# Kernel tuning notes

Hardware: AMD Instinct MI355X
Metric: run time of the kernel (lower is better)

Reference implementation:

```python
import jax, jax.numpy as jnp
import numpy as np

B, D, CTX, H = 262144, 16, 128, 192
IN_DIM = D + CTX + 1  # 145


def _linear_init(k, fan_in, fan_out):
    bound = 1.0 / np.sqrt(fan_in)
    kw, kb = jax.random.split(k)
    W = jax.random.uniform(kw, (fan_in, fan_out), jnp.float32, -bound, bound)
    b = jax.random.uniform(kb, (fan_out,), jnp.float32, -bound, bound)
    return W, b


def setup_inputs() -> dict:
    key = jax.random.key(0)
    ks = jax.random.split(key, 7)
    W1, b1 = _linear_init(ks[0], IN_DIM, H)
    W2, b2 = _linear_init(ks[1], H, H)
    W3, b3 = _linear_init(ks[2], H, D)
    return {
        "t": jax.random.uniform(ks[3], (), jnp.float32),
        "y": jax.random.normal(ks[4], (B, D), jnp.float32),
        "logp": jnp.zeros((B,), jnp.float32),
        "h": jax.random.normal(ks[5], (B, CTX), jnp.float32),
        "eps": jax.random.normal(ks[6], (B, D), jnp.float32),
        "W1": W1, "b1": b1, "W2": W2, "b2": b2, "W3": W3, "b3": b3,
    }


def _mlp(x, W1, b1, W2, b2, W3, b3):
    # 3-layer MLP, exact (erf) GELU as torch.nn.GELU default
    x = jax.nn.gelu(x @ W1 + b1, approximate=False)
    x = jax.nn.gelu(x @ W2 + b2, approximate=False)
    return x @ W3 + b3


def reference(t, y, logp, h, eps, W1, b1, W2, b2, W3, b3):
    Bsz = y.shape[0]
    t_feat = jnp.ones((Bsz, 1), y.dtype) * t

    def f_of_y(yy):
        inp = jnp.concatenate([yy, h, t_feat], axis=1)  # (B, D+CTX+1)
        return _mlp(inp, W1, b1, W2, b2, W3, b3)  # (B, D)

    # Hutchinson: torch computes g = J^T eps then (g*eps).sum(1) = eps^T J^T eps,
    # which per-row equals eps^T J eps = dot(eps, J eps). Forward-mode JVP computes
    # f and J eps in one fused pass (same math, no explicit backward graph).
    f, Jeps = jax.jvp(f_of_y, (y,), (eps,))
    trace = jnp.sum(Jeps * eps, axis=1)  # (B,)
    dlogp = -trace
    dh = jnp.zeros_like(h)
    return (f, dlogp, dh)
```

## Files before the change

### kernel.cpp

```cpp
#include <hip/hip_runtime.h>
#include <hip/hip_bf16.h>
#include <math.h>

#define B_TOTAL 262144
#define D 16
#define CTX 128
#define H 192
#define IN_DIM 145
#define KP1 160
#define M 32
#define BLOCK 256

typedef __attribute__((ext_vector_type(8))) short bf16x8;
typedef __attribute__((ext_vector_type(4))) float f32x4;
typedef __attribute__((ext_vector_type(4))) unsigned short u16x4;

#define MFMA(a, b, c) __builtin_amdgcn_mfma_f32_16x16x32_bf16((a), (b), (c), 0, 0, 0)

__device__ __forceinline__ unsigned short f2bf_rne(float f) {
    unsigned u = __builtin_bit_cast(unsigned, f);
    u += 0x7FFFu + ((u >> 16) & 1u);
    return (unsigned short)(u >> 16);
}
__device__ __forceinline__ void split2(float v, unsigned short& hi, unsigned short& lo) {
    unsigned u = __builtin_bit_cast(unsigned, v);
    hi = (unsigned short)(u >> 16);
    float hf = __builtin_bit_cast(float, u & 0xFFFF0000u);
    lo = f2bf_rne(v - hf);
}
__device__ __forceinline__ void gelu_pair(float x, float& a, float& gp) {
    float s   = x * x;
    float e   = __expf(-0.5f * s);
    float az  = fabsf(x) * 0.70710678118654752f;
    float t   = __builtin_amdgcn_rcpf(fmaf(0.3275911f, az, 1.0f));
    float p   = t * (0.254829592f + t * (-0.284496736f + t * (1.421413741f +
                t * (-1.453152027f + t * 1.061405429f))));
    float erfv = __builtin_copysignf(1.0f - p * e, x);
    float phi  = fmaf(0.5f, erfv, 0.5f);
    gp = fmaf(0.39894228040143268f * x, e, phi);
    a  = x * phi;
}

__global__ void prep_weights(const float* __restrict__ W1,
                             const float* __restrict__ W2,
                             const float* __restrict__ W3,
                             unsigned short* __restrict__ wt)
{
    int i = blockIdx.x * 256 + threadIdx.x;
    if (i < H * KP1) {
        int n = i / KP1, kp = i % KP1;
        float v = 0.0f;
        if (kp < 16)       v = W1[kp * H + n];
        else if (kp == 16) v = W1[144 * H + n];
        else if (kp >= 32) v = W1[(kp - 16) * H + n];
        wt[i] = f2bf_rne(v);
        return;
    }
    i -= H * KP1;
    if (i < H * H) {
        int n = i / H, k = i % H;
        wt[30720 + i] = f2bf_rne(W2[k * H + n]);
        return;
    }
    i -= H * H;
    if (i < D * H) {
        int n = i / H, k = i % H;
        wt[67584 + i] = f2bf_rne(W3[k * D + n]);
    }
}

__global__ __launch_bounds__(BLOCK, 4) void odefunc_mfma(
    const float* __restrict__ t_ptr,
    const float* __restrict__ y,
    const float* __restrict__ h,
    const float* __restrict__ eps,
    const float* __restrict__ b1,
    const float* __restrict__ b2,
    const float* __restrict__ b3,
    const unsigned short* __restrict__ wt,
    float* __restrict__ out_f,
    float* __restrict__ out_dlogp,
    float* __restrict__ out_dh)
{
    __shared__ __align__(16) unsigned char smem[25600];
    unsigned short (*Xh)[168] = (unsigned short (*)[168])(smem);
    unsigned short (*Xl)[40]  = (unsigned short (*)[40])(smem + 10752);
    unsigned short (*Th)[40]  = (unsigned short (*)[40])(smem + 13312);
    unsigned short (*Tl)[40]  = (unsigned short (*)[40])(smem + 15872);
    unsigned short (*A)[200]  = (unsigned short (*)[200])(smem);
    unsigned short (*U)[200]  = (unsigned short (*)[200])(smem + 12800);

    const int tid  = threadIdx.x;
    const int lane = tid & 63;
    const int wv   = tid >> 6;
    const int quad = lane >> 4;
    const int l16  = lane & 15;
    const size_t r0 = (size_t)blockIdx.x * M;

    const unsigned short* Wt1 = wt;
    const unsigned short* Wt2 = wt + 30720;
    const unsigned short* Wt3 = wt + 67584;

    {
        float4 z4 = {0.f, 0.f, 0.f, 0.f};
        #pragma unroll
        for (int i = 0; i < 4; ++i) {
            int idx = tid + i * BLOCK;
            int r = idx >> 5, c4 = (idx & 31) * 4;
            *(float4*)(out_dh + (r0 + r) * CTX + c4) = z4;
        }
    }

    {
        int task = tid >> 7, idx = tid & 127;
        int r = idx >> 2, d4 = (idx & 3) * 4;
        const float* src = task ? eps : y;
        float4 v = *(const float4*)(src + (r0 + r) * D + d4);
        ushort4 hi, lo;
        split2(v.x, hi.x, lo.x); split2(v.y, hi.y, lo.y);
        split2(v.z, hi.z, lo.z); split2(v.w, hi.w, lo.w);
        if (task == 0) { *(ushort4*)&Xh[r][d4] = hi; *(ushort4*)&Xl[r][d4] = lo; }
        else           { *(ushort4*)&Th[r][d4] = hi; *(ushort4*)&Tl[r][d4] = lo; }
    }
    if (tid < M) {
        int r = tid;
        float tv = t_ptr[0];
        unsigned short thi, tlo;
        split2(tv, thi, tlo);
        ushort4 z4 = {0, 0, 0, 0};
        ushort4 t4 = {thi, 0, 0, 0};
        ushort4 l4 = {tlo, 0, 0, 0};
        *(ushort4*)&Xh[r][16] = t4; *(ushort4*)&Xh[r][20] = z4;
        *(ushort4*)&Xh[r][24] = z4; *(ushort4*)&Xh[r][28] = z4;
        *(ushort4*)&Xl[r][16] = l4; *(ushort4*)&Xl[r][20] = z4;
        *(ushort4*)&Xl[r][24] = z4; *(ushort4*)&Xl[r][28] = z4;
        *(ushort4*)&Th[r][16] = z4; *(ushort4*)&Th[r][20] = z4;
        *(ushort4*)&Th[r][24] = z4; *(ushort4*)&Th[r][28] = z4;
        *(ushort4*)&Tl[r][16] = z4; *(ushort4*)&Tl[r][20] = z4;
        *(ushort4*)&Tl[r][24] = z4; *(ushort4*)&Tl[r][28] = z4;
    }
    #pragma unroll
    for (int i = 0; i < 4; ++i) {
        int idx = tid + i * BLOCK;
        int r = idx >> 5, c4 = (idx & 31) * 4;
        float4 v = *(const float4*)(h + (r0 + r) * CTX + c4);
        ushort4 hv = { f2bf_rne(v.x), f2bf_rne(v.y), f2bf_rne(v.z), f2bf_rne(v.w) };
        *(ushort4*)&Xh[r][32 + c4] = hv;
    }
    __syncthreads();

    const f32x4 zf = {0.f, 0.f, 0.f, 0.f};

    f32x4 z[2][3], u[2][3];
    #pragma unroll
    for (int rt = 0; rt < 2; ++rt)
        #pragma unroll
        for (int j = 0; j < 3; ++j) { z[rt][j] = zf; u[rt][j] = zf; }

    bf16x8 w1f[3][5];
    #pragma unroll
    for (int j = 0; j < 3; ++j) {
        int n = (wv * 3 + j) * 16 + l16;
        #pragma unroll
        for (int kc = 0; kc < 5; ++kc)
            w1f[j][kc] = *(const bf16x8*)(Wt1 + n * KP1 + kc * 32 + quad * 8);
    }
    #pragma unroll
    for (int kc = 0; kc < 5; ++kc)
        #pragma unroll
        for (int rt = 0; rt < 2; ++rt) {
            bf16x8 ah = *(const bf16x8*)&Xh[rt * 16 + l16][kc * 32 + quad * 8];
            #pragma unroll
            for (int j = 0; j < 3; ++j) z[rt][j] = MFMA(w1f[j][kc], ah, z[rt][j]);
        }
    #pragma unroll
    for (int rt = 0; rt < 2; ++rt) {
        int m = rt * 16 + l16;
        bf16x8 al = *(const bf16x8*)&Xl[m][quad * 8];
        bf16x8 th = *(const bf16x8*)&Th[m][quad * 8];
        bf16x8 tl = *(const bf16x8*)&Tl[m][quad * 8];
        #pragma unroll
        for (int j = 0; j < 3; ++j) {
            z[rt][j] = MFMA(w1f[j][0], al, z[rt][j]);
            u[rt][j] = MFMA(w1f[j][0], th, u[rt][j]);
            u[rt][j] = MFMA(w1f[j][0], tl, u[rt][j]);
        }
    }
    __syncthreads();
    #pragma unroll
    for (int j = 0; j < 3; ++j) {
        int n4 = (wv * 3 + j) * 16 + quad * 4;
        f32x4 bb4 = *(const f32x4*)(b1 + n4);
        #pragma unroll
        for (int rt = 0; rt < 2; ++rt) {
            int m = rt * 16 + l16;
            u16x4 a4, u4;
            #pragma unroll
            for (int rg = 0; rg < 4; ++rg) {
                float x = z[rt][j][rg] + bb4[rg];
                float a, gp; gelu_pair(x, a, gp);
                a4[rg] = f2bf_rne(a);
                u4[rg] = f2bf_rne(u[rt][j][rg] * gp);
            }
            *(u16x4*)&A[m][n4] = a4;
            *(u16x4*)&U[m][n4] = u4;
        }
    }
    __syncthreads();

    f32x4 z2[2][3], u2[2][3];
    #pragma unroll
    for (int rt = 0; rt < 2; ++rt)
        #pragma unroll
        for (int j = 0; j < 3; ++j) { z2[rt][j] = zf; u2[rt][j] = zf; }

    bf16x8 w2f[3][6];
    #pragma unroll
    for (int j = 0; j < 3; ++j) {
        int n = (wv * 3 + j) * 16 + l16;
        #pragma unroll
        for (int kc = 0; kc < 6; ++kc)
            w2f[j][kc] = *(const bf16x8*)(Wt2 + n * H + kc * 32 + quad * 8);
    }
    #pragma unroll
    for (int kc = 0; kc < 6; ++kc)
        #pragma unroll
        for (int rt = 0; rt < 2; ++rt) {
            int m = rt * 16 + l16, o = kc * 32 + quad * 8;
            bf16x8 av = *(const bf16x8*)&A[m][o];
            bf16x8 uv = *(const bf16x8*)&U[m][o];
            #pragma unroll
            for (int j = 0; j < 3; ++j) {
                z2[rt][j] = MFMA(w2f[j][kc], av, z2[rt][j]);
                u2[rt][j] = MFMA(w2f[j][kc], uv, u2[rt][j]);
            }
        }
    __syncthreads();
    #pragma unroll
    for (int j = 0; j < 3; ++j) {
        int n4 = (wv * 3 + j) * 16 + quad * 4;
        f32x4 bb4 = *(const f32x4*)(b2 + n4);
        #pragma unroll
        for (int rt = 0; rt < 2; ++rt) {
            int m = rt * 16 + l16;
            u16x4 a4, u4;
            #pragma unroll
            for (int rg = 0; rg < 4; ++rg) {
                float x = z2[rt][j][rg] + bb4[rg];
                float a, gp; gelu_pair(x, a, gp);
                a4[rg] = f2bf_rne(a);
                u4[rg] = f2bf_rne(u2[rt][j][rg] * gp);
            }
            *(u16x4*)&A[m][n4] = a4;
            *(u16x4*)&U[m][n4] = u4;
        }
    }
    __syncthreads();

    {
        const int strm = wv & 1, r3 = wv >> 1;
        const unsigned short (*P)[200] = strm ? U : A;

        bf16x8 w3f[6];
        #pragma unroll
        for (int kc = 0; kc < 6; ++kc)
            w3f[kc] = *(const bf16x8*)(Wt3 + l16 * H + kc * 32 + quad * 8);

        f32x4 acc = zf;
        #pragma unroll
        for (int kc = 0; kc < 6; ++kc) {
            bf16x8 xv = *(const bf16x8*)&P[r3 * 16 + l16][kc * 32 + quad * 8];
            acc = MFMA(w3f[kc], xv, acc);
        }

        const int m = r3 * 16 + l16;
        if (strm == 0) {
            f32x4 bb4 = *(const f32x4*)(b3 + quad * 4);
            f32x4 o = acc + bb4;
            *(f32x4*)(out_f + (r0 + m) * D + quad * 4) = o;
        } else {
            f32x4 e4 = *(const f32x4*)(eps + (r0 + m) * D + quad * 4);
            float pr = acc[0] * e4[0] + acc[1] * e4[1] + acc[2] * e4[2] + acc[3] * e4[3];
            pr += __shfl_xor(pr, 16, 64);
            pr += __shfl_xor(pr, 32, 64);
            if (quad == 0)
                out_dlogp[r0 + m] = -pr;
        }
    }
}

extern "C" void kernel_launch(void* const* d_in, const int* in_sizes, int n_in,
                              void* d_out, int out_size, void* d_ws, size_t ws_size,
                              hipStream_t stream)
{
    const float* t   = (const float*)d_in[0];
    const float* y   = (const float*)d_in[1];
    const float* h   = (const float*)d_in[3];
    const float* eps = (const float*)d_in[4];
    const float* W1  = (const float*)d_in[5];
    const float* b1  = (const float*)d_in[6];
    const float* W2  = (const float*)d_in[7];
    const float* b2  = (const float*)d_in[8];
    const float* W3  = (const float*)d_in[9];
    const float* b3  = (const float*)d_in[10];

    float* out       = (float*)d_out;
    float* out_f     = out;
    float* out_dlogp = out + (size_t)B_TOTAL * D;
    float* out_dh    = out + (size_t)B_TOTAL * (D + 1);

    unsigned short* wt = (unsigned short*)d_ws;

    int prep_elems = H * KP1 + H * H + D * H;
    prep_weights<<<(prep_elems + 255) / 256, 256, 0, stream>>>(W1, W2, W3, wt);

    odefunc_mfma<<<B_TOTAL / M, BLOCK, 0, stream>>>(
        t, y, h, eps, b1, b2, b3, wt, out_f, out_dlogp, out_dh);
}
```

Before: 394.0 us.

## Make MLP kernel persistent with register prefetch of next tile inputs

Converts the one-tile-per-block launch into a persistent grid of 1024 blocks that loop over row tiles. Each iteration prefetches the next tile's y/eps and h values into registers while the current tile computes, overlapping global loads with MFMA work. Shared memory is split into separate non-aliased arrays, and launch bounds drop from 4 to 3 blocks per CU, which allows more registers but may cut occupancy. The t-feature padding is written once outside the loop.

New measurement: 525.1 us. 1.33x slower.

```diff
diff --git a/kernel.cpp b/kernel.cpp
--- a/kernel.cpp
+++ b/kernel.cpp
@@ -10,6 +10,8 @@
 #define KP1 160
 #define M 32
 #define BLOCK 256
+#define NT (B_TOTAL / M)
+#define GRID 1024
 
 typedef __attribute__((ext_vector_type(8))) short bf16x8;
 typedef __attribute__((ext_vector_type(4))) float f32x4;
@@ -69,7 +71,7 @@
     }
 }
 
-__global__ __launch_bounds__(BLOCK, 4) void odefunc_mfma(
+__global__ __launch_bounds__(BLOCK, 3) void odefunc_mfma(
     const float* __restrict__ t_ptr,
     const float* __restrict__ y,
     const float* __restrict__ h,
@@ -82,46 +84,21 @@
     float* __restrict__ out_dlogp,
     float* __restrict__ out_dh)
 {
-    __shared__ __align__(16) unsigned char smem[25600];
-    unsigned short (*Xh)[168] = (unsigned short (*)[168])(smem);
-    unsigned short (*Xl)[40]  = (unsigned short (*)[40])(smem + 10752);
-    unsigned short (*Th)[40]  = (unsigned short (*)[40])(smem + 13312);
-    unsigned short (*Tl)[40]  = (unsigned short (*)[40])(smem + 15872);
-    unsigned short (*A)[200]  = (unsigned short (*)[200])(smem);
-    unsigned short (*U)[200]  = (unsigned short (*)[200])(smem + 12800);
+    __shared__ __align__(16) unsigned short Xh[M][168];
+    __shared__ __align__(16) unsigned short Xl[M][40];
+    __shared__ __align__(16) unsigned short Th[M][40], Tl[M][40];
+    __shared__ __align__(16) unsigned short A[M][200], U[M][200];
 
     const int tid  = threadIdx.x;
     const int lane = tid & 63;
     const int wv   = tid >> 6;
     const int quad = lane >> 4;
     const int l16  = lane & 15;
-    const size_t r0 = (size_t)blockIdx.x * M;
 
     const unsigned short* Wt1 = wt;
     const unsigned short* Wt2 = wt + 30720;
     const unsigned short* Wt3 = wt + 67584;
 
-    {
-        float4 z4 = {0.f, 0.f, 0.f, 0.f};
-        #pragma unroll
-        for (int i = 0; i < 4; ++i) {
-            int idx = tid + i * BLOCK;
-            int r = idx >> 5, c4 = (idx & 31) * 4;
-            *(float4*)(out_dh + (r0 + r) * CTX + c4) = z4;
-        }
-    }
-
-    {
-        int task = tid >> 7, idx = tid & 127;
-        int r = idx >> 2, d4 = (idx & 3) * 4;
-        const float* src = task ? eps : y;
-        float4 v = *(const float4*)(src + (r0 + r) * D + d4);
-        ushort4 hi, lo;
-        split2(v.x, hi.x, lo.x); split2(v.y, hi.y, lo.y);
-        split2(v.z, hi.z, lo.z); split2(v.w, hi.w, lo.w);
-        if (task == 0) { *(ushort4*)&Xh[r][d4] = hi; *(ushort4*)&Xl[r][d4] = lo; }
-        else           { *(ushort4*)&Th[r][d4] = hi; *(ushort4*)&Tl[r][d4] = lo; }
-    }
     if (tid < M) {
         int r = tid;
         float tv = t_ptr[0];
@@ -139,152 +116,200 @@
         *(ushort4*)&Tl[r][16] = z4; *(ushort4*)&Tl[r][20] = z4;
         *(ushort4*)&Tl[r][24] = z4; *(ushort4*)&Tl[r][28] = z4;
     }
-    #pragma unroll
-    for (int i = 0; i < 4; ++i) {
-        int idx = tid + i * BLOCK;
-        int r = idx >> 5, c4 = (idx & 31) * 4;
-        float4 v = *(const float4*)(h + (r0 + r) * CTX + c4);
-        ushort4 hv = { f2bf_rne(v.x), f2bf_rne(v.y), f2bf_rne(v.z), f2bf_rne(v.w) };
-        *(ushort4*)&Xh[r][32 + c4] = hv;
-    }
-    __syncthreads();
+
+    const int task = tid >> 7, sidx = tid & 127;
+    const int sr = sidx >> 2, sd4 = (sidx & 3) * 4;
+    const float* ye_src = task ? eps : y;
+    const int hrb = tid >> 5, hc = (tid & 31) * 4;
+
+    float4 pf_ye, pf_h0, pf_h1, pf_h2, pf_h3;
+    {
+        const size_t r0 = (size_t)blockIdx.x * M;
+        pf_ye = *(const float4*)(ye_src + (r0 + sr) * D + sd4);
+        pf_h0 = *(const float4*)(h + (r0 + hrb     ) * CTX + hc);
+        pf_h1 = *(const float4*)(h + (r0 + hrb +  8) * CTX + hc);
+        pf_h2 = *(const float4*)(h + (r0 + hrb + 16) * CTX + hc);
+        pf_h3 = *(const float4*)(h + (r0 + hrb + 24) * CTX + hc);
+    }
 
     const f32x4 zf = {0.f, 0.f, 0.f, 0.f};
 
-    f32x4 z[2][3], u[2][3];
-    #pragma unroll
-    for (int rt = 0; rt < 2; ++rt)
-        #pragma unroll
-        for (int j = 0; j < 3; ++j) { z[rt][j] = zf; u[rt][j] = zf; }
-
-    bf16x8 w1f[3][5];
-    #pragma unroll
-    for (int j = 0; j < 3; ++j) {
-        int n = (wv * 3 + j) * 16 + l16;
+    for (int it = blockIdx.x; it < NT; it += GRID) {
+        const size_t r0 = (size_t)it * M;
+
+        {
+            float4 z4 = {0.f, 0.f, 0.f, 0.f};
+            #pragma unroll
+            for (int i = 0; i < 4; ++i) {
+                int idx = tid + i * BLOCK;
+                int r = idx >> 5, c4 = (idx & 31) * 4;
+                *(float4*)(out_dh + (r0 + r) * CTX + c4) = z4;
+            }
+        }
+
+        {
+            ushort4 hi, lo;
+            split2(pf_ye.x, hi.x, lo.x); split2(pf_ye.y, hi.y, lo.y);
+            split2(pf_ye.z, hi.z, lo.z); split2(pf_ye.w, hi.w, lo.w);
+            if (task == 0) { *(ushort4*)&Xh[sr][sd4] = hi; *(ushort4*)&Xl[sr][sd4] = lo; }
+            else           { *(ushort4*)&Th[sr][sd4] = hi; *(ushort4*)&Tl[sr][sd4] = lo; }
+
+            ushort4 hv;
+            hv = (ushort4){ f2bf_rne(pf_h0.x), f2bf_rne(pf_h0.y), f2bf_rne(pf_h0.z), f2bf_rne(pf_h0.w) };
+            *(ushort4*)&Xh[hrb     ][32 + hc] = hv;
+            hv = (ushort4){ f2bf_rne(pf_h1.x), f2bf_rne(pf_h1.y), f2bf_rne(pf_h1.z), f2bf_rne(pf_h1.w) };
+            *(ushort4*)&Xh[hrb +  8][32 + hc] = hv;
+            hv = (ushort4){ f2bf_rne(pf_h2.x), f2bf_rne(pf_h2.y), f2bf_rne(pf_h2.z), f2bf_rne(pf_h2.w) };
+            *(ushort4*)&Xh[hrb + 16][32 + hc] = hv;
+            hv = (ushort4){ f2bf_rne(pf_h3.x), f2bf_rne(pf_h3.y), f2bf_rne(pf_h3.z), f2bf_rne(pf_h3.w) };
+            *(ushort4*)&Xh[hrb + 24][32 + hc] = hv;
+        }
+
+        if (it + GRID < NT) {
+            const size_t rn = (size_t)(it + GRID) * M;
+            pf_ye = *(const float4*)(ye_src + (rn + sr) * D + sd4);
+            pf_h0 = *(const float4*)(h + (rn + hrb     ) * CTX + hc);
+            pf_h1 = *(const float4*)(h + (rn + hrb +  8) * CTX + hc);
+            pf_h2 = *(const float4*)(h + (rn + hrb + 16) * CTX + hc);
+            pf_h3 = *(const float4*)(h + (rn + hrb + 24) * CTX + hc);
+        }
+
+        __syncthreads();
+
+        f32x4 z[2][3], u[2][3];
+        #pragma unroll
+        for (int rt = 0; rt < 2; ++rt)
+            #pragma unroll
+            for (int j = 0; j < 3; ++j) { z[rt][j] = zf; u[rt][j] = zf; }
+
+        bf16x8 w1f[3][5];
+        #pragma unroll
+        for (int j = 0; j < 3; ++j) {
+            int n = (wv * 3 + j) * 16 + l16;
+            #pragma unroll
+            for (int kc = 0; kc < 5; ++kc)
+                w1f[j][kc] = *(const bf16x8*)(Wt1 + n * KP1 + kc * 32 + quad * 8);
+        }
         #pragma unroll
         for (int kc = 0; kc < 5; ++kc)
-            w1f[j][kc] = *(const bf16x8*)(Wt1 + n * KP1 + kc * 32 + quad * 8);
-    }
-    #pragma unroll
-    for (int kc = 0; kc < 5; ++kc)
-        #pragma unroll
-        for (int rt = 0; rt < 2; ++rt) {
-            bf16x8 ah = *(const bf16x8*)&Xh[rt * 16 + l16][kc * 32 + quad * 8];
-            #pragma unroll
-            for (int j = 0; j < 3; ++j) z[rt][j] = MFMA(w1f[j][kc], ah, z[rt][j]);
-        }
-    #pragma unroll
-    for (int rt = 0; rt < 2; ++rt) {
-        int m = rt * 16 + l16;
-        bf16x8 al = *(const bf16x8*)&Xl[m][quad * 8];
-        bf16x8 th = *(const bf16x8*)&Th[m][quad * 8];
-        bf16x8 tl = *(const bf16x8*)&Tl[m][quad * 8];
-        #pragma unroll
-        for (int j = 0; j < 3; ++j) {
-            z[rt][j] = MFMA(w1f[j][0], al, z[rt][j]);
-            u[rt][j] = MFMA(w1f[j][0], th, u[rt][j]);
-            u[rt][j] = MFMA(w1f[j][0], tl, u[rt][j]);
-        }
-    }
-    __syncthreads();
-    #pragma unroll
-    for (int j = 0; j < 3; ++j) {
-        int n4 = (wv * 3 + j) * 16 + quad * 4;
-        f32x4 bb4 = *(const f32x4*)(b1 + n4);
+            #pragma unroll
+            for (int rt = 0; rt < 2; ++rt) {
+                bf16x8 ah = *(const bf16x8*)&Xh[rt * 16 + l16][kc * 32 + quad * 8];
+                #pragma unroll
+                for (int j = 0; j < 3; ++j) z[rt][j] = MFMA(w1f[j][kc], ah, z[rt][j]);
+            }
         #pragma unroll
         for (int rt = 0; rt < 2; ++rt) {
             int m = rt * 16 + l16;
-            u16x4 a4, u4;
-            #pragma unroll
-            for (int rg = 0; rg < 4; ++rg) {
-                float x = z[rt][j][rg] + bb4[rg];
-                float a, gp; gelu_pair(x, a, gp);
-                a4[rg] = f2bf_rne(a);
-                u4[rg] = f2bf_rne(u[rt][j][rg] * gp);
-            }
-            *(u16x4*)&A[m][n4] = a4;
-            *(u16x4*)&U[m][n4] = u4;
-        }
-    }
-    __syncthreads();
-
-    f32x4 z2[2][3], u2[2][3];
-    #pragma unroll
-    for (int rt = 0; rt < 2; ++rt)
-        #pragma unroll
-        for (int j = 0; j < 3; ++j) { z2[rt][j] = zf; u2[rt][j] = zf; }
-
-    bf16x8 w2f[3][6];
-    #pragma unroll
-    for (int j = 0; j < 3; ++j) {
-        int n = (wv * 3 + j) * 16 + l16;
+            bf16x8 al = *(const bf16x8*)&Xl[m][quad * 8];
+            bf16x8 th = *(const bf16x8*)&Th[m][quad * 8];
+            bf16x8 tl = *(const bf16x8*)&Tl[m][quad * 8];
+            #pragma unroll
+            for (int j = 0; j < 3; ++j) {
+                z[rt][j] = MFMA(w1f[j][0], al, z[rt][j]);
+                u[rt][j] = MFMA(w1f[j][0], th, u[rt][j]);
+                u[rt][j] = MFMA(w1f[j][0], tl, u[rt][j]);
+            }
+        }
+        #pragma unroll
+        for (int j = 0; j < 3; ++j) {
+            int n4 = (wv * 3 + j) * 16 + quad * 4;
+            f32x4 bb4 = *(const f32x4*)(b1 + n4);
+            #pragma unroll
+            for (int rt = 0; rt < 2; ++rt) {
+                int m = rt * 16 + l16;
+                u16x4 a4, u4;
+                #pragma unroll
+                for (int rg = 0; rg < 4; ++rg) {
+                    float x = z[rt][j][rg] + bb4[rg];
+                    float a, gp; gelu_pair(x, a, gp);
+                    a4[rg] = f2bf_rne(a);
+                    u4[rg] = f2bf_rne(u[rt][j][rg] * gp);
+                }
+                *(u16x4*)&A[m][n4] = a4;
+                *(u16x4*)&U[m][n4] = u4;
+            }
+        }
+        __syncthreads();
+
+        f32x4 z2[2][3], u2[2][3];
+        #pragma unroll
+        for (int rt = 0; rt < 2; ++rt)
+            #pragma unroll
+            for (int j = 0; j < 3; ++j) { z2[rt][j] = zf; u2[rt][j] = zf; }
+
+        bf16x8 w2f[3][6];
+        #pragma unroll
+        for (int j = 0; j < 3; ++j) {
+            int n = (wv * 3 + j) * 16 + l16;
+            #pragma unroll
+            for (int kc = 0; kc < 6; ++kc)
+                w2f[j][kc] = *(const bf16x8*)(Wt2 + n * H + kc * 32 + quad * 8);
+        }
         #pragma unroll
         for (int kc = 0; kc < 6; ++kc)
-            w2f[j][kc] = *(const bf16x8*)(Wt2 + n * H + kc * 32 + quad * 8);
-    }
-    #pragma unroll
-    for (int kc = 0; kc < 6; ++kc)
-        #pragma unroll
-        for (int rt = 0; rt < 2; ++rt) {
-            int m = rt * 16 + l16, o = kc * 32 + quad * 8;
-            bf16x8 av = *(const bf16x8*)&A[m][o];
-            bf16x8 uv = *(const bf16x8*)&U[m][o];
-            #pragma unroll
-            for (int j = 0; j < 3; ++j) {
-                z2[rt][j] = MFMA(w2f[j][kc], av, z2[rt][j]);
-                u2[rt][j] = MFMA(w2f[j][kc], uv, u2[rt][j]);
-            }
-        }
-    __syncthreads();
-    #pragma unroll
-    for (int j = 0; j < 3; ++j) {
-        int n4 = (wv * 3 + j) * 16 + quad * 4;
-        f32x4 bb4 = *(const f32x4*)(b2 + n4);
-        #pragma unroll
-        for (int rt = 0; rt < 2; ++rt) {
-            int m = rt * 16 + l16;
-            u16x4 a4, u4;
-            #pragma unroll
-            for (int rg = 0; rg < 4; ++rg) {
-                float x = z2[rt][j][rg] + bb4[rg];
-                float a, gp; gelu_pair(x, a, gp);
-                a4[rg] = f2bf_rne(a);
-                u4[rg] = f2bf_rne(u2[rt][j][rg] * gp);
-            }
-            *(u16x4*)&A[m][n4] = a4;
-            *(u16x4*)&U[m][n4] = u4;
-        }
-    }
-    __syncthreads();
-
-    {
-        const int strm = wv & 1, r3 = wv >> 1;
-        const unsigned short (*P)[200] = strm ? U : A;
-
-        bf16x8 w3f[6];
-        #pragma unroll
-        for (int kc = 0; kc < 6; ++kc)
-            w3f[kc] = *(const bf16x8*)(Wt3 + l16 * H + kc * 32 + quad * 8);
-
-        f32x4 acc = zf;
-        #pragma unroll
-        for (int kc = 0; kc < 6; ++kc) {
-            bf16x8 xv = *(const bf16x8*)&P[r3 * 16 + l16][kc * 32 + quad * 8];
-            acc = MFMA(w3f[kc], xv, acc);
-        }
-
-        const int m = r3 * 16 + l16;
-        if (strm == 0) {
-            f32x4 bb4 = *(const f32x4*)(b3 + quad * 4);
-            f32x4 o = acc + bb4;
-            *(f32x4*)(out_f + (r0 + m) * D + quad * 4) = o;
-        } else {
-            f32x4 e4 = *(const f32x4*)(eps + (r0 + m) * D + quad * 4);
-            float pr = acc[0] * e4[0] + acc[1] * e4[1] + acc[2] * e4[2] + acc[3] * e4[3];
-            pr += __shfl_xor(pr, 16, 64);
-            pr += __shfl_xor(pr, 32, 64);
-            if (quad == 0)
-                out_dlogp[r0 + m] = -pr;
+            #pragma unroll
+            for (int rt = 0; rt < 2; ++rt) {
+                int m = rt * 16 + l16, o = kc * 32 + quad * 8;
+                bf16x8 av = *(const bf16x8*)&A[m][o];
+                bf16x8 uv = *(const bf16x8*)&U[m][o];
+                #pragma unroll
+                for (int j = 0; j < 3; ++j) {
+                    z2[rt][j] = MFMA(w2f[j][kc], av, z2[rt][j]);
+                    u2[rt][j] = MFMA(w2f[j][kc], uv, u2[rt][j]);
+                }
+            }
+        __syncthreads();
+        #pragma unroll
+        for (int j = 0; j < 3; ++j) {
+            int n4 = (wv * 3 + j) * 16 + quad * 4;
+            f32x4 bb4 = *(const f32x4*)(b2 + n4);
+            #pragma unroll
+            for (int rt = 0; rt < 2; ++rt) {
+                int m = rt * 16 + l16;
+                u16x4 a4, u4;
+                #pragma unroll
+                for (int rg = 0; rg < 4; ++rg) {
+                    float x = z2[rt][j][rg] + bb4[rg];
+                    float a, gp; gelu_pair(x, a, gp);
+                    a4[rg] = f2bf_rne(a);
+                    u4[rg] = f2bf_rne(u2[rt][j][rg] * gp);
+                }
+                *(u16x4*)&A[m][n4] = a4;
+                *(u16x4*)&U[m][n4] = u4;
+            }
+        }
+        __syncthreads();
+
+        {
+            const int strm = wv & 1, r3 = wv >> 1;
+            const unsigned short (*P)[200] = strm ? U : A;
+
+            bf16x8 w3f[6];
+            #pragma unroll
+            for (int kc = 0; kc < 6; ++kc)
+                w3f[kc] = *(const bf16x8*)(Wt3 + l16 * H + kc * 32 + quad * 8);
+
+            f32x4 acc = zf;
+            #pragma unroll
+            for (int kc = 0; kc < 6; ++kc) {
+                bf16x8 xv = *(const bf16x8*)&P[r3 * 16 + l16][kc * 32 + quad * 8];
+                acc = MFMA(w3f[kc], xv, acc);
+            }
+
+            const int m = r3 * 16 + l16;
+            if (strm == 0) {
+                f32x4 bb4 = *(const f32x4*)(b3 + quad * 4);
+                f32x4 o = acc + bb4;
+                *(f32x4*)(out_f + (r0 + m) * D + quad * 4) = o;
+            } else {
+                f32x4 e4 = *(const f32x4*)(eps + (r0 + m) * D + quad * 4);
+                float pr = acc[0] * e4[0] + acc[1] * e4[1] + acc[2] * e4[2] + acc[3] * e4[3];
+                pr += __shfl_xor(pr, 16, 64);
+                pr += __shfl_xor(pr, 32, 64);
+                if (quad == 0)
+                    out_dlogp[r0 + m] = -pr;
+            }
         }
     }
 }
@@ -314,6 +339,6 @@
     int prep_elems = H * KP1 + H * H + D * H;
     prep_weights<<<(prep_elems + 255) / 256, 256, 0, stream>>>(W1, W2, W3, wt);
 
-    odefunc_mfma<<<B_TOTAL / M, BLOCK, 0, stream>>>(
+    odefunc_mfma<<<GRID, BLOCK, 0, stream>>>(
         t, y, h, eps, b1, b2, b3, wt, out_f, out_dlogp, out_dh);
 }
```

## Split each 32-row tile across 8 waves by row-half and column group

Applied to the files above, without the earlier changes.

Doubles the block to 512 threads. Each wave now handles one 16-row half and a third of the hidden columns, instead of both row tiles. This halves per-wave MFMA chains and accumulator registers and adds more waves to hide latency. In exchange, every wave reloads its full weight fragments, so per-block weight traffic doubles, and the final layer uses only half the waves.

Result: slower. 478.1 us (+21.4%).

```diff
diff --git a/kernel.cpp b/kernel.cpp
--- a/kernel.cpp
+++ b/kernel.cpp
@@ -9,7 +9,7 @@
 #define IN_DIM 145
 #define KP1 160
 #define M 32
-#define BLOCK 256
+#define BLOCK 512
 
 typedef __attribute__((ext_vector_type(8))) short bf16x8;
 typedef __attribute__((ext_vector_type(4))) float f32x4;
@@ -95,6 +95,8 @@
     const int wv   = tid >> 6;
     const int quad = lane >> 4;
     const int l16  = lane & 15;
+    const int rw   = wv >> 2;
+    const int cw   = wv & 3;
     const size_t r0 = (size_t)blockIdx.x * M;
 
     const unsigned short* Wt1 = wt;
@@ -104,14 +106,14 @@
     {
         float4 z4 = {0.f, 0.f, 0.f, 0.f};
         #pragma unroll
-        for (int i = 0; i < 4; ++i) {
+        for (int i = 0; i < 2; ++i) {
             int idx = tid + i * BLOCK;
             int r = idx >> 5, c4 = (idx & 31) * 4;
             *(float4*)(out_dh + (r0 + r) * CTX + c4) = z4;
         }
     }
 
-    {
+    if (tid < 256) {
         int task = tid >> 7, idx = tid & 127;
         int r = idx >> 2, d4 = (idx & 3) * 4;
         const float* src = task ? eps : y;
@@ -140,7 +142,7 @@
         *(ushort4*)&Tl[r][24] = z4; *(ushort4*)&Tl[r][28] = z4;
     }
     #pragma unroll
-    for (int i = 0; i < 4; ++i) {
+    for (int i = 0; i < 2; ++i) {
         int idx = tid + i * BLOCK;
         int r = idx >> 5, c4 = (idx & 31) * 4;
         float4 v = *(const float4*)(h + (r0 + r) * CTX + c4);
@@ -151,113 +153,98 @@
 
     const f32x4 zf = {0.f, 0.f, 0.f, 0.f};
 
-    f32x4 z[2][3], u[2][3];
-    #pragma unroll
-    for (int rt = 0; rt < 2; ++rt)
-        #pragma unroll
-        for (int j = 0; j < 3; ++j) { z[rt][j] = zf; u[rt][j] = zf; }
+    f32x4 z[3], u[3];
+    #pragma unroll
+    for (int j = 0; j < 3; ++j) { z[j] = zf; u[j] = zf; }
 
     bf16x8 w1f[3][5];
     #pragma unroll
     for (int j = 0; j < 3; ++j) {
-        int n = (wv * 3 + j) * 16 + l16;
+        int n = (cw * 3 + j) * 16 + l16;
         #pragma unroll
         for (int kc = 0; kc < 5; ++kc)
             w1f[j][kc] = *(const bf16x8*)(Wt1 + n * KP1 + kc * 32 + quad * 8);
     }
     #pragma unroll
-    for (int kc = 0; kc < 5; ++kc)
-        #pragma unroll
-        for (int rt = 0; rt < 2; ++rt) {
-            bf16x8 ah = *(const bf16x8*)&Xh[rt * 16 + l16][kc * 32 + quad * 8];
-            #pragma unroll
-            for (int j = 0; j < 3; ++j) z[rt][j] = MFMA(w1f[j][kc], ah, z[rt][j]);
-        }
-    #pragma unroll
-    for (int rt = 0; rt < 2; ++rt) {
-        int m = rt * 16 + l16;
+    for (int kc = 0; kc < 5; ++kc) {
+        bf16x8 ah = *(const bf16x8*)&Xh[rw * 16 + l16][kc * 32 + quad * 8];
+        #pragma unroll
+        for (int j = 0; j < 3; ++j) z[j] = MFMA(w1f[j][kc], ah, z[j]);
+    }
+    {
+        int m = rw * 16 + l16;
         bf16x8 al = *(const bf16x8*)&Xl[m][quad * 8];
         bf16x8 th = *(const bf16x8*)&Th[m][quad * 8];
         bf16x8 tl = *(const bf16x8*)&Tl[m][quad * 8];
         #pragma unroll
         for (int j = 0; j < 3; ++j) {
-            z[rt][j] = MFMA(w1f[j][0], al, z[rt][j]);
-            u[rt][j] = MFMA(w1f[j][0], th, u[rt][j]);
-            u[rt][j] = MFMA(w1f[j][0], tl, u[rt][j]);
+            z[j] = MFMA(w1f[j][0], al, z[j]);
+            u[j] = MFMA(w1f[j][0], th, u[j]);
+            u[j] = MFMA(w1f[j][0], tl, u[j]);
         }
     }
     __syncthreads();
     #pragma unroll
     for (int j = 0; j < 3; ++j) {
-        int n4 = (wv * 3 + j) * 16 + quad * 4;
+        int n4 = (cw * 3 + j) * 16 + quad * 4;
         f32x4 bb4 = *(const f32x4*)(b1 + n4);
-        #pragma unroll
-        for (int rt = 0; rt < 2; ++rt) {
-            int m = rt * 16 + l16;
-            u16x4 a4, u4;
-            #pragma unroll
-            for (int rg = 0; rg < 4; ++rg) {
-                float x = z[rt][j][rg] + bb4[rg];
-                float a, gp; gelu_pair(x, a, gp);
-                a4[rg] = f2bf_rne(a);
-                u4[rg] = f2bf_rne(u[rt][j][rg] * gp);
-            }
-            *(u16x4*)&A[m][n4] = a4;
-            *(u16x4*)&U[m][n4] = u4;
-        }
-    }
-    __syncthreads();
-
-    f32x4 z2[2][3], u2[2][3];
-    #pragma unroll
-    for (int rt = 0; rt < 2; ++rt)
-        #pragma unroll
-        for (int j = 0; j < 3; ++j) { z2[rt][j] = zf; u2[rt][j] = zf; }
+        int m = rw * 16 + l16;
+        u16x4 a4, u4;
+        #pragma unroll
+        for (int rg = 0; rg < 4; ++rg) {
+            float x = z[j][rg] + bb4[rg];
+            float a, gp; gelu_pair(x, a, gp);
+            a4[rg] = f2bf_rne(a);
+            u4[rg] = f2bf_rne(u[j][rg] * gp);
+        }
+        *(u16x4*)&A[m][n4] = a4;
+        *(u16x4*)&U[m][n4] = u4;
+    }
+    __syncthreads();
+
+    f32x4 z2[3], u2[3];
+    #pragma unroll
+    for (int j = 0; j < 3; ++j) { z2[j] = zf; u2[j] = zf; }
 
     bf16x8 w2f[3][6];
     #pragma unroll
     for (int j = 0; j < 3; ++j) {
-        int n = (wv * 3 + j) * 16 + l16;
+        int n = (cw * 3 + j) * 16 + l16;
         #pragma unroll
         for (int kc = 0; kc < 6; ++kc)
             w2f[j][kc] = *(const bf16x8*)(Wt2 + n * H + kc * 32 + quad * 8);
     }
     #pragma unroll
-    for (int kc = 0; kc < 6; ++kc)
-        #pragma unroll
-        for (int rt = 0; rt < 2; ++rt) {
-            int m = rt * 16 + l16, o = kc * 32 + quad * 8;
-            bf16x8 av = *(const bf16x8*)&A[m][o];
-            bf16x8 uv = *(const bf16x8*)&U[m][o];
-            #pragma unroll
-            for (int j = 0; j < 3; ++j) {
-                z2[rt][j] = MFMA(w2f[j][kc], av, z2[rt][j]);
-                u2[rt][j] = MFMA(w2f[j][kc], uv, u2[rt][j]);
-            }
-        }
+    for (int kc = 0; kc < 6; ++kc) {
+        int m = rw * 16 + l16, o = kc * 32 + quad * 8;
+        bf16x8 av = *(const bf16x8*)&A[m][o];
+        bf16x8 uv = *(const bf16x8*)&U[m][o];
+        #pragma unroll
+        for (int j = 0; j < 3; ++j) {
+            z2[j] = MFMA(w2f[j][kc], av, z2[j]);
+            u2[j] = MFMA(w2f[j][kc], uv, u2[j]);
+        }
+    }
     __syncthreads();
     #pragma unroll
     for (int j = 0; j < 3; ++j) {
-        int n4 = (wv * 3 + j) * 16 + quad * 4;
+        int n4 = (cw * 3 + j) * 16 + quad * 4;
         f32x4 bb4 = *(const f32x4*)(b2 + n4);
-        #pragma unroll
-        for (int rt = 0; rt < 2; ++rt) {
-            int m = rt * 16 + l16;
-            u16x4 a4, u4;
-            #pragma unroll
-            for (int rg = 0; rg < 4; ++rg) {
-                float x = z2[rt][j][rg] + bb4[rg];
-                float a, gp; gelu_pair(x, a, gp);
-                a4[rg] = f2bf_rne(a);
-                u4[rg] = f2bf_rne(u2[rt][j][rg] * gp);
-            }
-            *(u16x4*)&A[m][n4] = a4;
-            *(u16x4*)&U[m][n4] = u4;
-        }
-    }
-    __syncthreads();
-
-    {
+        int m = rw * 16 + l16;
+        u16x4 a4, u4;
+        #pragma unroll
+        for (int rg = 0; rg < 4; ++rg) {
+            float x = z2[j][rg] + bb4[rg];
+            float a, gp; gelu_pair(x, a, gp);
+            a4[rg] = f2bf_rne(a);
+            u4[rg] = f2bf_rne(u2[j][rg] * gp);
+        }
+        *(u16x4*)&A[m][n4] = a4;
+        *(u16x4*)&U[m][n4] = u4;
+    }
+    __syncthreads();
+
+    if (wv < 4) {
         const int strm = wv & 1, r3 = wv >> 1;
         const unsigned short (*P)[200] = strm ? U : A;
 
```
